# Optimization experiments

Hardware: AMD Instinct MI355X
Metric: run time of the kernel (lower is better)

## Reference

```python
import jax, jax.numpy as jnp
import numpy as np
import math

D_MODEL = 256

def setup_inputs() -> dict:
    key = jax.random.key(0)
    k1, k2, k3, k4 = jax.random.split(key, 4)
    Nq, Nh, d = 512, 100000, D_MODEL
    query_embed = jax.random.normal(k1, (Nq, d), dtype=jnp.float32)
    key_embed = jax.random.normal(k2, (Nh, d), dtype=jnp.float32)
    value_embed = jax.random.normal(k3, (Nh, d), dtype=jnp.float32)
    mask_proposals = jax.random.uniform(k4, (Nq, Nh), dtype=jnp.float32)
    return {"query_embed": query_embed, "key_embed": key_embed,
            "value_embed": value_embed, "mask_proposals": mask_proposals}

def reference(query_embed, key_embed, value_embed, mask_proposals):
    # [Nq, Nh] scores: QK^T / sqrt(d) + log(mask)
    scale = 1.0 / math.sqrt(D_MODEL)
    scores = jnp.einsum('qd,hd->qh', query_embed, key_embed) * scale
    scores = scores + jnp.log(mask_proposals)
    attn = jax.nn.softmax(scores, axis=-1)
    return jnp.einsum('qh,hd->qd', attn, value_embed)
```

## Files before the change

### kernel.cpp

```cpp
#include <hip/hip_runtime.h>
#include <hip/hip_bf16.h>

typedef __attribute__((ext_vector_type(8))) short short8;
typedef __attribute__((ext_vector_type(4))) float floatx4;
typedef __attribute__((ext_vector_type(4))) unsigned short ushort4v;

#define NQ 512
#define NH 100000
#define DM 256
#define BH 64

#define KSTR 264
#define VSTR 72
#define WSTR 72

#define MFMA_BF16(a, b, c) __builtin_amdgcn_mfma_f32_16x16x32_bf16((a), (b), (c), 0, 0, 0)

__device__ __forceinline__ unsigned short f2bf(float f) {
    union { float f; unsigned u; } v; v.f = f;
    unsigned u = v.u + 0x7fffu + ((v.u >> 16) & 1u);
    return (unsigned short)(u >> 16);
}

__global__ __launch_bounds__(512, 2)
void maskattn_phase1(const float* __restrict__ Qg,
                     const float* __restrict__ Kg,
                     const float* __restrict__ Vg,
                     const float* __restrict__ Mg,
                     float* __restrict__ numW,
                     float* __restrict__ denW,
                     int CH)
{
    __shared__ __attribute__((aligned(16))) unsigned short K_lds[64 * KSTR];
    __shared__ __attribute__((aligned(16))) unsigned short V_lds[256 * VSTR];
    __shared__ __attribute__((aligned(16))) unsigned short w_lds[128 * WSTR];
    __shared__ float den_lds[2][128];

    const int tid  = threadIdx.x;
    const int lane = tid & 63;
    const int wid  = tid >> 6;
    const int wm   = wid >> 1;
    const int wn   = wid & 1;
    const int g    = lane >> 4;
    const int l15  = lane & 15;

    const int qt    = blockIdx.x & 3;
    const int hc    = blockIdx.x >> 2;
    const int qbase = qt * 128;
    const long h0   = (long)hc * CH;
    const long hEnd = (h0 + CH < (long)NH) ? (h0 + CH) : (long)NH;

    short8 qa[2][8];
#pragma unroll
    for (int fq = 0; fq < 2; ++fq) {
        const float* qp = Qg + (size_t)(qbase + 32*wm + 16*fq + l15) * DM + 8*g;
#pragma unroll
        for (int ks = 0; ks < 8; ++ks) {
            floatx4 a = *(const floatx4*)(qp + 32*ks);
            floatx4 b = *(const floatx4*)(qp + 32*ks + 4);
            short8 fr;
            fr[0]=(short)f2bf(a[0]); fr[1]=(short)f2bf(a[1]);
            fr[2]=(short)f2bf(a[2]); fr[3]=(short)f2bf(a[3]);
            fr[4]=(short)f2bf(b[0]); fr[5]=(short)f2bf(b[1]);
            fr[6]=(short)f2bf(b[2]); fr[7]=(short)f2bf(b[3]);
            qa[fq][ks] = fr;
        }
    }

    floatx4 acc[2][8];
#pragma unroll
    for (int i = 0; i < 2; ++i)
#pragma unroll
        for (int j = 0; j < 8; ++j) {
            floatx4 z = {0.f, 0.f, 0.f, 0.f};
            acc[i][j] = z;
        }
    float dacc[8];
#pragma unroll
    for (int i = 0; i < 8; ++i) dacc[i] = 0.f;

    const int ntiles = (hEnd > h0) ? (int)((hEnd - h0 + BH - 1) / BH) : 0;

    for (int t = 0; t < ntiles; ++t) {
        const long hb = h0 + (long)t * BH;

        {
            const int hr = tid >> 3;
            const int d0 = (tid & 7) * 4;
            long krow = hb + hr; if (krow > (long)NH - 1) krow = (long)NH - 1;
            const float* kp = Kg + (size_t)krow * DM;
#pragma unroll
            for (int c = 0; c < 8; ++c) {
                const int d = d0 + 32*c;
                floatx4 v = *(const floatx4*)(kp + d);
                ushort4v p;
                p[0]=f2bf(v[0]); p[1]=f2bf(v[1]); p[2]=f2bf(v[2]); p[3]=f2bf(v[3]);
                *(ushort4v*)&K_lds[hr*KSTR + d] = p;
            }
        }
        {
            const int dcol = tid & 63;
            const int hq0  = tid >> 6;
#pragma unroll
            for (int jh = 0; jh < 2; ++jh) {
                const int hq = hq0 + 8*jh;
#pragma unroll
                for (int jd = 0; jd < 4; ++jd) {
                    const int d = dcol + 64*jd;
                    ushort4v p;
#pragma unroll
                    for (int r = 0; r < 4; ++r) {
                        long hrow = hb + 4*hq + r; if (hrow > (long)NH - 1) hrow = (long)NH - 1;
                        p[r] = f2bf(Vg[(size_t)hrow * DM + d]);
                    }
                    *(ushort4v*)&V_lds[d*VSTR + 4*hq] = p;
                }
            }
        }
        __syncthreads();

        floatx4 sf[2][2];
        {
            floatx4 z = {0.f, 0.f, 0.f, 0.f};
            sf[0][0]=z; sf[0][1]=z; sf[1][0]=z; sf[1][1]=z;
        }
#pragma unroll
        for (int ks = 0; ks < 8; ++ks) {
            short8 kb0 = *(const short8*)&K_lds[(32*wn +      l15)*KSTR + 32*ks + 8*g];
            short8 kb1 = *(const short8*)&K_lds[(32*wn + 16 + l15)*KSTR + 32*ks + 8*g];
            sf[0][0] = MFMA_BF16(qa[0][ks], kb0, sf[0][0]);
            sf[0][1] = MFMA_BF16(qa[0][ks], kb1, sf[0][1]);
            sf[1][0] = MFMA_BF16(qa[1][ks], kb0, sf[1][0]);
            sf[1][1] = MFMA_BF16(qa[1][ks], kb1, sf[1][1]);
        }

#pragma unroll
        for (int fn = 0; fn < 2; ++fn) {
            const long h = hb + 32*wn + 16*fn + l15;
            const bool valid = (h < hEnd);
#pragma unroll
            for (int fq = 0; fq < 2; ++fq) {
#pragma unroll
                for (int j = 0; j < 4; ++j) {
                    const int rloc = 32*wm + 16*fq + 4*g + j;
                    float m = valid ? Mg[(size_t)(qbase + rloc) * NH + h] : 0.f;
                    float s = sf[fq][fn][j] * 0.0625f;
                    s = (s > 60.f) ? 60.f : s;
                    float w = m * __expf(s);
                    dacc[fq*4 + j] += w;
                    w_lds[rloc*WSTR + 32*wn + 16*fn + l15] = f2bf(w);
                }
            }
        }
        __syncthreads();

#pragma unroll
        for (int ks = 0; ks < 2; ++ks) {
            short8 wa0 = *(const short8*)&w_lds[(32*wm +      l15)*WSTR + 32*ks + 8*g];
            short8 wa1 = *(const short8*)&w_lds[(32*wm + 16 + l15)*WSTR + 32*ks + 8*g];
#pragma unroll
            for (int fd = 0; fd < 8; ++fd) {
                short8 vb = *(const short8*)&V_lds[(128*wn + 16*fd + l15)*VSTR + 32*ks + 8*g];
                acc[0][fd] = MFMA_BF16(wa0, vb, acc[0][fd]);
                acc[1][fd] = MFMA_BF16(wa1, vb, acc[1][fd]);
            }
        }
        __syncthreads();
    }

#pragma unroll
    for (int r = 0; r < 8; ++r) {
        float v = dacc[r];
        v += __shfl_xor(v, 1);
        v += __shfl_xor(v, 2);
        v += __shfl_xor(v, 4);
        v += __shfl_xor(v, 8);
        if (l15 == 0) {
            const int fq = r >> 2, j = r & 3;
            den_lds[wn][32*wm + 16*fq + 4*g + j] = v;
        }
    }
    __syncthreads();
    if (tid < 128) {
        denW[(size_t)hc * NQ + qbase + tid] = den_lds[0][tid] + den_lds[1][tid];
    }

#pragma unroll
    for (int fq = 0; fq < 2; ++fq)
#pragma unroll
        for (int fd = 0; fd < 8; ++fd)
#pragma unroll
            for (int j = 0; j < 4; ++j) {
                const int qrow = qbase + 32*wm + 16*fq + 4*g + j;
                const int d    = 128*wn + 16*fd + l15;
                numW[((size_t)hc * NQ + qrow) * DM + d] = acc[fq][fd][j];
            }
}

__global__ void maskattn_reduce(const float* __restrict__ numW,
                                const float* __restrict__ denW,
                                float* __restrict__ out, int C)
{
    const int q = blockIdx.x;
    const int d = threadIdx.x;
    float sn = 0.f, sd = 0.f;
    for (int c = 0; c < C; ++c) {
        sn += numW[((size_t)c * NQ + q) * DM + d];
        sd += denW[(size_t)c * NQ + q];
    }
    out[(size_t)q * DM + d] = sn / sd;
}

extern "C" void kernel_launch(void* const* d_in, const int* in_sizes, int n_in,
                              void* d_out, int out_size, void* d_ws, size_t ws_size,
                              hipStream_t stream)
{
    const float* Qg = (const float*)d_in[0];
    const float* Kg = (const float*)d_in[1];
    const float* Vg = (const float*)d_in[2];
    const float* Mg = (const float*)d_in[3];
    float* out = (float*)d_out;

    const size_t per_chunk = (size_t)NQ * DM * sizeof(float) + (size_t)NQ * sizeof(float);
    int C = (int)(ws_size / per_chunk);
    if (C > 64) C = 64;
    float* numW;
    float* denW;
    if (C >= 1) {
        numW = (float*)d_ws;
        denW = numW + (size_t)C * NQ * DM;
    } else {
        C = 1;
        numW = out;
        denW = (float*)d_ws;
    }
    const int ch64 = (NH + 64*C - 1) / (64*C);
    const int CH = 64 * ch64;

    maskattn_phase1<<<dim3(4 * C), dim3(512), 0, stream>>>(Qg, Kg, Vg, Mg, numW, denW, CH);
    maskattn_reduce<<<dim3(NQ), dim3(DM), 0, stream>>>(numW, denW, out, C);
}
```

Before: 265.9 us.

## Shrink query tile to 64, swizzle LDS, prefetch mask, remap blocks

Query tile per block drops from 128 to 64 rows, so the grid has 8*C blocks instead of 4*C and each wave owns a single 16-row query fragment. Launch bounds move to 4 blocks per CU to raise occupancy. Padded LDS strides become XOR swizzles, which cuts LDS size and avoids bank conflicts. Mask values are loaded into registers before the K/V staging so their latency overlaps, and block IDs are remapped so neighbouring blocks share hidden chunks. The trade-off is that every K/V tile is now loaded and converted twice as often across query tiles, doubling that global traffic.

```diff
diff --git a/kernel.cpp b/kernel.cpp
--- a/kernel.cpp
+++ b/kernel.cpp
@@ -9,10 +9,7 @@
 #define NH 100000
 #define DM 256
 #define BH 64
-
-#define KSTR 264
-#define VSTR 72
-#define WSTR 72
+#define BQ 64
 
 #define MFMA_BF16(a, b, c) __builtin_amdgcn_mfma_f32_16x16x32_bf16((a), (b), (c), 0, 0, 0)
 
@@ -22,67 +19,85 @@
     return (unsigned short)(u >> 16);
 }
 
-__global__ __launch_bounds__(512, 2)
+__device__ __forceinline__ int kidx(int h, int d) { return (h * 256 + d) ^ ((h & 7) << 3); }
+__device__ __forceinline__ int vidx(int d, int h) { return (d * 64 + h) ^ ((d & 7) << 3); }
+__device__ __forceinline__ int widx(int q, int h) { return (q * 64 + h) ^ ((q & 7) << 3); }
+
+__global__ __launch_bounds__(512, 4)
 void maskattn_phase1(const float* __restrict__ Qg,
                      const float* __restrict__ Kg,
                      const float* __restrict__ Vg,
                      const float* __restrict__ Mg,
                      float* __restrict__ numW,
                      float* __restrict__ denW,
-                     int CH)
+                     int CH, int C)
 {
-    __shared__ __attribute__((aligned(16))) unsigned short K_lds[64 * KSTR];
-    __shared__ __attribute__((aligned(16))) unsigned short V_lds[256 * VSTR];
-    __shared__ __attribute__((aligned(16))) unsigned short w_lds[128 * WSTR];
-    __shared__ float den_lds[2][128];
+    __shared__ __attribute__((aligned(16))) unsigned short K_lds[64 * 256];
+    __shared__ __attribute__((aligned(16))) unsigned short V_lds[256 * 64];
+    __shared__ __attribute__((aligned(16))) unsigned short w_lds[64 * 64];
 
     const int tid  = threadIdx.x;
     const int lane = tid & 63;
     const int wid  = tid >> 6;
-    const int wm   = wid >> 1;
+    const int wq   = wid >> 1;
     const int wn   = wid & 1;
     const int g    = lane >> 4;
     const int l15  = lane & 15;
 
-    const int qt    = blockIdx.x & 3;
-    const int hc    = blockIdx.x >> 2;
-    const int qbase = qt * 128;
+    const int bid = blockIdx.x;
+    int qt, hc;
+    if ((C & 7) == 0) {
+        const int x = bid & 7;
+        const int r = bid >> 3;
+        qt = r & 7;
+        hc = x * (C >> 3) + (r >> 3);
+    } else {
+        qt = bid & 7;
+        hc = bid >> 3;
+    }
+    const int qbase = qt * BQ;
     const long h0   = (long)hc * CH;
     const long hEnd = (h0 + CH < (long)NH) ? (h0 + CH) : (long)NH;
 
-    short8 qa[2][8];
-#pragma unroll
-    for (int fq = 0; fq < 2; ++fq) {
-        const float* qp = Qg + (size_t)(qbase + 32*wm + 16*fq + l15) * DM + 8*g;
+    short8 qa[8];
+    {
+        const float* qp = Qg + (size_t)(qbase + 16 * wq + l15) * DM + 8 * g;
 #pragma unroll
         for (int ks = 0; ks < 8; ++ks) {
-            floatx4 a = *(const floatx4*)(qp + 32*ks);
-            floatx4 b = *(const floatx4*)(qp + 32*ks + 4);
+            floatx4 a = *(const floatx4*)(qp + 32 * ks);
+            floatx4 b = *(const floatx4*)(qp + 32 * ks + 4);
             short8 fr;
             fr[0]=(short)f2bf(a[0]); fr[1]=(short)f2bf(a[1]);
             fr[2]=(short)f2bf(a[2]); fr[3]=(short)f2bf(a[3]);
             fr[4]=(short)f2bf(b[0]); fr[5]=(short)f2bf(b[1]);
             fr[6]=(short)f2bf(b[2]); fr[7]=(short)f2bf(b[3]);
-            qa[fq][ks] = fr;
-        }
-    }
-
-    floatx4 acc[2][8];
-#pragma unroll
-    for (int i = 0; i < 2; ++i)
-#pragma unroll
-        for (int j = 0; j < 8; ++j) {
-            floatx4 z = {0.f, 0.f, 0.f, 0.f};
-            acc[i][j] = z;
-        }
-    float dacc[8];
-#pragma unroll
-    for (int i = 0; i < 8; ++i) dacc[i] = 0.f;
+            qa[ks] = fr;
+        }
+    }
+
+    floatx4 acc[8];
+#pragma unroll
+    for (int i = 0; i < 8; ++i) {
+        floatx4 z = {0.f, 0.f, 0.f, 0.f};
+        acc[i] = z;
+    }
+    float dacc[4] = {0.f, 0.f, 0.f, 0.f};
 
     const int ntiles = (hEnd > h0) ? (int)((hEnd - h0 + BH - 1) / BH) : 0;
 
     for (int t = 0; t < ntiles; ++t) {
         const long hb = h0 + (long)t * BH;
+
+        float mreg[2][4];
+#pragma unroll
+        for (int fn = 0; fn < 2; ++fn) {
+            const long h = hb + 32 * wn + 16 * fn + l15;
+            const bool valid = (h < hEnd);
+#pragma unroll
+            for (int j = 0; j < 4; ++j) {
+                mreg[fn][j] = valid ? Mg[(size_t)(qbase + 16 * wq + 4 * g + j) * NH + h] : 0.f;
+            }
+        }
 
         {
             const int hr = tid >> 3;
@@ -91,11 +106,11 @@
             const float* kp = Kg + (size_t)krow * DM;
 #pragma unroll
             for (int c = 0; c < 8; ++c) {
-                const int d = d0 + 32*c;
+                const int d = d0 + 32 * c;
                 floatx4 v = *(const floatx4*)(kp + d);
                 ushort4v p;
                 p[0]=f2bf(v[0]); p[1]=f2bf(v[1]); p[2]=f2bf(v[2]); p[3]=f2bf(v[3]);
-                *(ushort4v*)&K_lds[hr*KSTR + d] = p;
+                *(ushort4v*)&K_lds[kidx(hr, d)] = p;
             }
         }
         {
@@ -103,98 +118,85 @@
             const int hq0  = tid >> 6;
 #pragma unroll
             for (int jh = 0; jh < 2; ++jh) {
-                const int hq = hq0 + 8*jh;
+                const int hq = hq0 + 8 * jh;
 #pragma unroll
                 for (int jd = 0; jd < 4; ++jd) {
-                    const int d = dcol + 64*jd;
+                    const int d = dcol + 64 * jd;
                     ushort4v p;
 #pragma unroll
                     for (int r = 0; r < 4; ++r) {
-                        long hrow = hb + 4*hq + r; if (hrow > (long)NH - 1) hrow = (long)NH - 1;
+                        long hrow = hb + 4 * hq + r; if (hrow > (long)NH - 1) hrow = (long)NH - 1;
                         p[r] = f2bf(Vg[(size_t)hrow * DM + d]);
                     }
-                    *(ushort4v*)&V_lds[d*VSTR + 4*hq] = p;
+                    *(ushort4v*)&V_lds[vidx(d, 4 * hq)] = p;
                 }
             }
         }
         __syncthreads();
 
-        floatx4 sf[2][2];
+        floatx4 sf[2];
         {
             floatx4 z = {0.f, 0.f, 0.f, 0.f};
-            sf[0][0]=z; sf[0][1]=z; sf[1][0]=z; sf[1][1]=z;
+            sf[0] = z; sf[1] = z;
         }
 #pragma unroll
         for (int ks = 0; ks < 8; ++ks) {
-            short8 kb0 = *(const short8*)&K_lds[(32*wn +      l15)*KSTR + 32*ks + 8*g];
-            short8 kb1 = *(const short8*)&K_lds[(32*wn + 16 + l15)*KSTR + 32*ks + 8*g];
-            sf[0][0] = MFMA_BF16(qa[0][ks], kb0, sf[0][0]);
-            sf[0][1] = MFMA_BF16(qa[0][ks], kb1, sf[0][1]);
-            sf[1][0] = MFMA_BF16(qa[1][ks], kb0, sf[1][0]);
-            sf[1][1] = MFMA_BF16(qa[1][ks], kb1, sf[1][1]);
+            short8 kb0 = *(const short8*)&K_lds[kidx(32 * wn +      l15, 32 * ks + 8 * g)];
+            short8 kb1 = *(const short8*)&K_lds[kidx(32 * wn + 16 + l15, 32 * ks + 8 * g)];
+            sf[0] = MFMA_BF16(qa[ks], kb0, sf[0]);
+            sf[1] = MFMA_BF16(qa[ks], kb1, sf[1]);
         }
 
 #pragma unroll
         for (int fn = 0; fn < 2; ++fn) {
-            const long h = hb + 32*wn + 16*fn + l15;
-            const bool valid = (h < hEnd);
-#pragma unroll
-            for (int fq = 0; fq < 2; ++fq) {
-#pragma unroll
-                for (int j = 0; j < 4; ++j) {
-                    const int rloc = 32*wm + 16*fq + 4*g + j;
-                    float m = valid ? Mg[(size_t)(qbase + rloc) * NH + h] : 0.f;
-                    float s = sf[fq][fn][j] * 0.0625f;
-                    s = (s > 60.f) ? 60.f : s;
-                    float w = m * __expf(s);
-                    dacc[fq*4 + j] += w;
-                    w_lds[rloc*WSTR + 32*wn + 16*fn + l15] = f2bf(w);
-                }
+#pragma unroll
+            for (int j = 0; j < 4; ++j) {
+                const int rloc = 16 * wq + 4 * g + j;
+                float s = sf[fn][j] * 0.0625f;
+                s = (s > 60.f) ? 60.f : s;
+                float w = mreg[fn][j] * __expf(s);
+                dacc[j] += w;
+                w_lds[widx(rloc, 32 * wn + 16 * fn + l15)] = f2bf(w);
             }
         }
         __syncthreads();
 
 #pragma unroll
         for (int ks = 0; ks < 2; ++ks) {
-            short8 wa0 = *(const short8*)&w_lds[(32*wm +      l15)*WSTR + 32*ks + 8*g];
-            short8 wa1 = *(const short8*)&w_lds[(32*wm + 16 + l15)*WSTR + 32*ks + 8*g];
+            short8 wa = *(const short8*)&w_lds[widx(16 * wq + l15, 32 * ks + 8 * g)];
 #pragma unroll
             for (int fd = 0; fd < 8; ++fd) {
-                short8 vb = *(const short8*)&V_lds[(128*wn + 16*fd + l15)*VSTR + 32*ks + 8*g];
-                acc[0][fd] = MFMA_BF16(wa0, vb, acc[0][fd]);
-                acc[1][fd] = MFMA_BF16(wa1, vb, acc[1][fd]);
+                short8 vb = *(const short8*)&V_lds[vidx(128 * wn + 16 * fd + l15, 32 * ks + 8 * g)];
+                acc[fd] = MFMA_BF16(wa, vb, acc[fd]);
             }
         }
         __syncthreads();
     }
 
-#pragma unroll
-    for (int r = 0; r < 8; ++r) {
-        float v = dacc[r];
+    __syncthreads();
+    float* dshare = (float*)w_lds;
+#pragma unroll
+    for (int j = 0; j < 4; ++j) {
+        float v = dacc[j];
         v += __shfl_xor(v, 1);
         v += __shfl_xor(v, 2);
         v += __shfl_xor(v, 4);
         v += __shfl_xor(v, 8);
-        if (l15 == 0) {
-            const int fq = r >> 2, j = r & 3;
-            den_lds[wn][32*wm + 16*fq + 4*g + j] = v;
-        }
+        if (l15 == 0) dshare[wn * 64 + 16 * wq + 4 * g + j] = v;
     }
     __syncthreads();
-    if (tid < 128) {
-        denW[(size_t)hc * NQ + qbase + tid] = den_lds[0][tid] + den_lds[1][tid];
-    }
-
-#pragma unroll
-    for (int fq = 0; fq < 2; ++fq)
-#pragma unroll
-        for (int fd = 0; fd < 8; ++fd)
-#pragma unroll
-            for (int j = 0; j < 4; ++j) {
-                const int qrow = qbase + 32*wm + 16*fq + 4*g + j;
-                const int d    = 128*wn + 16*fd + l15;
-                numW[((size_t)hc * NQ + qrow) * DM + d] = acc[fq][fd][j];
-            }
+    if (tid < BQ) {
+        denW[(size_t)hc * NQ + qbase + tid] = dshare[tid] + dshare[64 + tid];
+    }
+
+#pragma unroll
+    for (int fd = 0; fd < 8; ++fd)
+#pragma unroll
+        for (int j = 0; j < 4; ++j) {
+            const int qrow = qbase + 16 * wq + 4 * g + j;
+            const int d    = 128 * wn + 16 * fd + l15;
+            numW[((size_t)hc * NQ + qrow) * DM + d] = acc[fd][j];
+        }
 }
 
 __global__ void maskattn_reduce(const float* __restrict__ numW,
@@ -234,9 +236,9 @@
         numW = out;
         denW = (float*)d_ws;
     }
-    const int ch64 = (NH + 64*C - 1) / (64*C);
+    const int ch64 = (NH + 64 * C - 1) / (64 * C);
     const int CH = 64 * ch64;
 
-    maskattn_phase1<<<dim3(4 * C), dim3(512), 0, stream>>>(Qg, Kg, Vg, Mg, numW, denW, CH);
+    maskattn_phase1<<<dim3((NQ / BQ) * C), dim3(512), 0, stream>>>(Qg, Kg, Vg, Mg, numW, denW, CH, C);
     maskattn_reduce<<<dim3(NQ), dim3(DM), 0, stream>>>(numW, denW, out, C);
 }
```

Measured after the change: 507.9 us. 1.91x slower.

## Double-buffer K/V tiles with register prefetch and XOR-swizzled LDS layout

Applied to the files above, without the earlier changes.

The K/V loads and mask loads for the next tile are now issued into registers before the current tile's two MFMA stages, then written to a second LDS buffer after the PV MFMAs. Global memory latency can then overlap with compute, and the previous per-tile load-then-sync stall goes away. Padded LDS strides are replaced by XOR swizzles to avoid bank conflicts. Blocks are also remapped so that consecutive block IDs spread across h-chunks. The cost is higher register pressure (kreg, vreg and two mask arrays) and double the K/V LDS, which may lower occupancy below the two blocks per CU requested by launch bounds.

```diff
diff --git a/kernel.cpp b/kernel.cpp
--- a/kernel.cpp
+++ b/kernel.cpp
@@ -9,10 +9,7 @@
 #define NH 100000
 #define DM 256
 #define BH 64
-
-#define KSTR 264
-#define VSTR 72
-#define WSTR 72
+#define BQ 128
 
 #define MFMA_BF16(a, b, c) __builtin_amdgcn_mfma_f32_16x16x32_bf16((a), (b), (c), 0, 0, 0)
 
@@ -20,6 +17,71 @@
     union { float f; unsigned u; } v; v.f = f;
     unsigned u = v.u + 0x7fffu + ((v.u >> 16) & 1u);
     return (unsigned short)(u >> 16);
+}
+
+__device__ __forceinline__ int kidx(int h, int d) { return (h * 256 + d) ^ ((h & 7) << 3); }
+__device__ __forceinline__ int vidx(int d, int h) { return (d * 64 + h) ^ ((d & 7) << 3); }
+__device__ __forceinline__ int widx(int q, int h) { return (q * 64 + h) ^ ((q & 7) << 3); }
+
+__device__ __forceinline__ void issue_kv(const float* __restrict__ Kg,
+                                         const float* __restrict__ Vg,
+                                         long hb, int tid,
+                                         floatx4* kreg, float* vreg)
+{
+    const int khr = tid >> 3, kd0 = (tid & 7) * 4;
+    long krow = hb + khr; if (krow > (long)NH - 1) krow = (long)NH - 1;
+    const float* kp = Kg + (size_t)krow * DM;
+#pragma unroll
+    for (int c = 0; c < 8; ++c) kreg[c] = *(const floatx4*)(kp + kd0 + 32 * c);
+
+    const int vd = tid & 63, vh0 = tid >> 6;
+#pragma unroll
+    for (int jh = 0; jh < 2; ++jh)
+#pragma unroll
+        for (int r = 0; r < 4; ++r) {
+            long vrow = hb + 4 * (vh0 + 8 * jh) + r; if (vrow > (long)NH - 1) vrow = (long)NH - 1;
+            const float* vp = Vg + (size_t)vrow * DM + vd;
+#pragma unroll
+            for (int jd = 0; jd < 4; ++jd)
+                vreg[jh * 16 + jd * 4 + r] = vp[64 * jd];
+        }
+}
+
+__device__ __forceinline__ void write_kv(unsigned short* Kb, unsigned short* Vb,
+                                         int tid, const floatx4* kreg, const float* vreg)
+{
+    const int khr = tid >> 3, kd0 = (tid & 7) * 4;
+#pragma unroll
+    for (int c = 0; c < 8; ++c) {
+        floatx4 v = kreg[c];
+        ushort4v p;
+        p[0] = f2bf(v[0]); p[1] = f2bf(v[1]); p[2] = f2bf(v[2]); p[3] = f2bf(v[3]);
+        *(ushort4v*)&Kb[kidx(khr, kd0 + 32 * c)] = p;
+    }
+    const int vd = tid & 63, vh0 = tid >> 6;
+#pragma unroll
+    for (int jh = 0; jh < 2; ++jh)
+#pragma unroll
+        for (int jd = 0; jd < 4; ++jd) {
+            ushort4v p;
+#pragma unroll
+            for (int r = 0; r < 4; ++r) p[r] = f2bf(vreg[jh * 16 + jd * 4 + r]);
+            *(ushort4v*)&Vb[vidx(vd + 64 * jd, 4 * (vh0 + 8 * jh))] = p;
+        }
+}
+
+__device__ __forceinline__ void issue_mask(const float* __restrict__ Mg, long hb,
+                                           int qrow0, int wn, int g, int l15, float* m)
+{
+#pragma unroll
+    for (int fn = 0; fn < 2; ++fn) {
+        long h = hb + 32 * wn + 16 * fn + l15; if (h > (long)NH - 1) h = (long)NH - 1;
+#pragma unroll
+        for (int fq = 0; fq < 2; ++fq)
+#pragma unroll
+            for (int j = 0; j < 4; ++j)
+                m[fn * 8 + fq * 4 + j] = Mg[(size_t)(qrow0 + 16 * fq + 4 * g + j) * NH + h];
+    }
 }
 
 __global__ __launch_bounds__(512, 2)
@@ -29,12 +91,11 @@
                      const float* __restrict__ Mg,
                      float* __restrict__ numW,
                      float* __restrict__ denW,
-                     int CH)
-{
-    __shared__ __attribute__((aligned(16))) unsigned short K_lds[64 * KSTR];
-    __shared__ __attribute__((aligned(16))) unsigned short V_lds[256 * VSTR];
-    __shared__ __attribute__((aligned(16))) unsigned short w_lds[128 * WSTR];
-    __shared__ float den_lds[2][128];
+                     int CH, int C)
+{
+    __shared__ __attribute__((aligned(16))) unsigned short K_lds[2][64 * 256];
+    __shared__ __attribute__((aligned(16))) unsigned short V_lds[2][64 * 256];
+    __shared__ __attribute__((aligned(16))) unsigned short w_lds[128 * 64];
 
     const int tid  = threadIdx.x;
     const int lane = tid & 63;
@@ -44,20 +105,30 @@
     const int g    = lane >> 4;
     const int l15  = lane & 15;
 
-    const int qt    = blockIdx.x & 3;
-    const int hc    = blockIdx.x >> 2;
-    const int qbase = qt * 128;
+    const int bid = blockIdx.x;
+    int qt, hc;
+    if ((C & 7) == 0) {
+        const int x = bid & 7;
+        const int r = bid >> 3;
+        qt = r & 3;
+        hc = x * (C >> 3) + (r >> 2);
+    } else {
+        qt = bid & 3;
+        hc = bid >> 2;
+    }
+    const int qbase = qt * BQ;
     const long h0   = (long)hc * CH;
     const long hEnd = (h0 + CH < (long)NH) ? (h0 + CH) : (long)NH;
+    const int qrow0 = qbase + 32 * wm;
 
     short8 qa[2][8];
 #pragma unroll
     for (int fq = 0; fq < 2; ++fq) {
-        const float* qp = Qg + (size_t)(qbase + 32*wm + 16*fq + l15) * DM + 8*g;
+        const float* qp = Qg + (size_t)(qrow0 + 16 * fq + l15) * DM + 8 * g;
 #pragma unroll
         for (int ks = 0; ks < 8; ++ks) {
-            floatx4 a = *(const floatx4*)(qp + 32*ks);
-            floatx4 b = *(const floatx4*)(qp + 32*ks + 4);
+            floatx4 a = *(const floatx4*)(qp + 32 * ks);
+            floatx4 b = *(const floatx4*)(qp + 32 * ks + 4);
             short8 fr;
             fr[0]=(short)f2bf(a[0]); fr[1]=(short)f2bf(a[1]);
             fr[2]=(short)f2bf(a[2]); fr[3]=(short)f2bf(a[3]);
@@ -71,103 +142,85 @@
 #pragma unroll
     for (int i = 0; i < 2; ++i)
 #pragma unroll
-        for (int j = 0; j < 8; ++j) {
-            floatx4 z = {0.f, 0.f, 0.f, 0.f};
-            acc[i][j] = z;
-        }
+        for (int j = 0; j < 8; ++j) { floatx4 z = {0.f,0.f,0.f,0.f}; acc[i][j] = z; }
     float dacc[8];
 #pragma unroll
     for (int i = 0; i < 8; ++i) dacc[i] = 0.f;
 
     const int ntiles = (hEnd > h0) ? (int)((hEnd - h0 + BH - 1) / BH) : 0;
 
-    for (int t = 0; t < ntiles; ++t) {
-        const long hb = h0 + (long)t * BH;
-
-        {
-            const int hr = tid >> 3;
-            const int d0 = (tid & 7) * 4;
-            long krow = hb + hr; if (krow > (long)NH - 1) krow = (long)NH - 1;
-            const float* kp = Kg + (size_t)krow * DM;
-#pragma unroll
-            for (int c = 0; c < 8; ++c) {
-                const int d = d0 + 32*c;
-                floatx4 v = *(const floatx4*)(kp + d);
-                ushort4v p;
-                p[0]=f2bf(v[0]); p[1]=f2bf(v[1]); p[2]=f2bf(v[2]); p[3]=f2bf(v[3]);
-                *(ushort4v*)&K_lds[hr*KSTR + d] = p;
-            }
-        }
-        {
-            const int dcol = tid & 63;
-            const int hq0  = tid >> 6;
-#pragma unroll
-            for (int jh = 0; jh < 2; ++jh) {
-                const int hq = hq0 + 8*jh;
-#pragma unroll
-                for (int jd = 0; jd < 4; ++jd) {
-                    const int d = dcol + 64*jd;
-                    ushort4v p;
-#pragma unroll
-                    for (int r = 0; r < 4; ++r) {
-                        long hrow = hb + 4*hq + r; if (hrow > (long)NH - 1) hrow = (long)NH - 1;
-                        p[r] = f2bf(Vg[(size_t)hrow * DM + d]);
+    if (ntiles > 0) {
+        floatx4 kreg[8];
+        float   vreg[32];
+        float   mcur[16], mnext[16];
+
+        issue_kv(Kg, Vg, h0, tid, kreg, vreg);
+        issue_mask(Mg, h0, qrow0, wn, g, l15, mcur);
+        write_kv(K_lds[0], V_lds[0], tid, kreg, vreg);
+        __syncthreads();
+
+        int cur = 0;
+        for (int t = 0; t < ntiles; ++t) {
+            const long hb = h0 + (long)t * BH;
+
+            issue_kv(Kg, Vg, hb + BH, tid, kreg, vreg);
+            issue_mask(Mg, hb + BH, qrow0, wn, g, l15, mnext);
+
+            const unsigned short* Kc = K_lds[cur];
+            floatx4 sf[2][2];
+            { floatx4 z = {0.f,0.f,0.f,0.f}; sf[0][0]=z; sf[0][1]=z; sf[1][0]=z; sf[1][1]=z; }
+#pragma unroll
+            for (int ks = 0; ks < 8; ++ks) {
+                short8 kb0 = *(const short8*)&Kc[kidx(32 * wn +      l15, 32 * ks + 8 * g)];
+                short8 kb1 = *(const short8*)&Kc[kidx(32 * wn + 16 + l15, 32 * ks + 8 * g)];
+                sf[0][0] = MFMA_BF16(qa[0][ks], kb0, sf[0][0]);
+                sf[0][1] = MFMA_BF16(qa[0][ks], kb1, sf[0][1]);
+                sf[1][0] = MFMA_BF16(qa[1][ks], kb0, sf[1][0]);
+                sf[1][1] = MFMA_BF16(qa[1][ks], kb1, sf[1][1]);
+            }
+
+#pragma unroll
+            for (int fn = 0; fn < 2; ++fn) {
+                const long h = hb + 32 * wn + 16 * fn + l15;
+                const bool valid = (h < hEnd);
+#pragma unroll
+                for (int fq = 0; fq < 2; ++fq)
+#pragma unroll
+                    for (int j = 0; j < 4; ++j) {
+                        const int rloc = 32 * wm + 16 * fq + 4 * g + j;
+                        float m = valid ? mcur[fn * 8 + fq * 4 + j] : 0.f;
+                        float s = sf[fq][fn][j] * 0.0625f;
+                        s = (s > 60.f) ? 60.f : s;
+                        float w = m * __expf(s);
+                        dacc[fq * 4 + j] += w;
+                        w_lds[widx(rloc, 32 * wn + 16 * fn + l15)] = f2bf(w);
                     }
-                    *(ushort4v*)&V_lds[d*VSTR + 4*hq] = p;
+            }
+            __syncthreads();
+
+            const unsigned short* Vc = V_lds[cur];
+#pragma unroll
+            for (int ks = 0; ks < 2; ++ks) {
+                short8 wa0 = *(const short8*)&w_lds[widx(32 * wm +      l15, 32 * ks + 8 * g)];
+                short8 wa1 = *(const short8*)&w_lds[widx(32 * wm + 16 + l15, 32 * ks + 8 * g)];
+#pragma unroll
+                for (int fd = 0; fd < 8; ++fd) {
+                    short8 vb = *(const short8*)&Vc[vidx(128 * wn + 16 * fd + l15, 32 * ks + 8 * g)];
+                    acc[0][fd] = MFMA_BF16(wa0, vb, acc[0][fd]);
+                    acc[1][fd] = MFMA_BF16(wa1, vb, acc[1][fd]);
                 }
             }
-        }
-        __syncthreads();
-
-        floatx4 sf[2][2];
-        {
-            floatx4 z = {0.f, 0.f, 0.f, 0.f};
-            sf[0][0]=z; sf[0][1]=z; sf[1][0]=z; sf[1][1]=z;
-        }
-#pragma unroll
-        for (int ks = 0; ks < 8; ++ks) {
-            short8 kb0 = *(const short8*)&K_lds[(32*wn +      l15)*KSTR + 32*ks + 8*g];
-            short8 kb1 = *(const short8*)&K_lds[(32*wn + 16 + l15)*KSTR + 32*ks + 8*g];
-            sf[0][0] = MFMA_BF16(qa[0][ks], kb0, sf[0][0]);
-            sf[0][1] = MFMA_BF16(qa[0][ks], kb1, sf[0][1]);
-            sf[1][0] = MFMA_BF16(qa[1][ks], kb0, sf[1][0]);
-            sf[1][1] = MFMA_BF16(qa[1][ks], kb1, sf[1][1]);
-        }
-
-#pragma unroll
-        for (int fn = 0; fn < 2; ++fn) {
-            const long h = hb + 32*wn + 16*fn + l15;
-            const bool valid = (h < hEnd);
-#pragma unroll
-            for (int fq = 0; fq < 2; ++fq) {
-#pragma unroll
-                for (int j = 0; j < 4; ++j) {
-                    const int rloc = 32*wm + 16*fq + 4*g + j;
-                    float m = valid ? Mg[(size_t)(qbase + rloc) * NH + h] : 0.f;
-                    float s = sf[fq][fn][j] * 0.0625f;
-                    s = (s > 60.f) ? 60.f : s;
-                    float w = m * __expf(s);
-                    dacc[fq*4 + j] += w;
-                    w_lds[rloc*WSTR + 32*wn + 16*fn + l15] = f2bf(w);
-                }
-            }
-        }
-        __syncthreads();
-
-#pragma unroll
-        for (int ks = 0; ks < 2; ++ks) {
-            short8 wa0 = *(const short8*)&w_lds[(32*wm +      l15)*WSTR + 32*ks + 8*g];
-            short8 wa1 = *(const short8*)&w_lds[(32*wm + 16 + l15)*WSTR + 32*ks + 8*g];
-#pragma unroll
-            for (int fd = 0; fd < 8; ++fd) {
-                short8 vb = *(const short8*)&V_lds[(128*wn + 16*fd + l15)*VSTR + 32*ks + 8*g];
-                acc[0][fd] = MFMA_BF16(wa0, vb, acc[0][fd]);
-                acc[1][fd] = MFMA_BF16(wa1, vb, acc[1][fd]);
-            }
-        }
-        __syncthreads();
-    }
-
+
+            write_kv(K_lds[cur ^ 1], V_lds[cur ^ 1], tid, kreg, vreg);
+#pragma unroll
+            for (int i = 0; i < 16; ++i) mcur[i] = mnext[i];
+            __syncthreads();
+            cur ^= 1;
+        }
+    }
+
+    __syncthreads();
+    float* dshare = (float*)w_lds;
 #pragma unroll
     for (int r = 0; r < 8; ++r) {
         float v = dacc[r];
@@ -177,12 +230,12 @@
         v += __shfl_xor(v, 8);
         if (l15 == 0) {
             const int fq = r >> 2, j = r & 3;
-            den_lds[wn][32*wm + 16*fq + 4*g + j] = v;
+            dshare[wn * 128 + 32 * wm + 16 * fq + 4 * g + j] = v;
         }
     }
     __syncthreads();
-    if (tid < 128) {
-        denW[(size_t)hc * NQ + qbase + tid] = den_lds[0][tid] + den_lds[1][tid];
+    if (tid < BQ) {
+        denW[(size_t)hc * NQ + qbase + tid] = dshare[tid] + dshare[128 + tid];
     }
 
 #pragma unroll
@@ -191,8 +244,8 @@
         for (int fd = 0; fd < 8; ++fd)
 #pragma unroll
             for (int j = 0; j < 4; ++j) {
-                const int qrow = qbase + 32*wm + 16*fq + 4*g + j;
-                const int d    = 128*wn + 16*fd + l15;
+                const int qrow = qbase + 32 * wm + 16 * fq + 4 * g + j;
+                const int d    = 128 * wn + 16 * fd + l15;
                 numW[((size_t)hc * NQ + qrow) * DM + d] = acc[fq][fd][j];
             }
 }
@@ -234,9 +287,9 @@
         numW = out;
         denW = (float*)d_ws;
     }
-    const int ch64 = (NH + 64*C - 1) / (64*C);
+    const int ch64 = (NH + 64 * C - 1) / (64 * C);
     const int CH = 64 * ch64;
 
-    maskattn_phase1<<<dim3(4 * C), dim3(512), 0, stream>>>(Qg, Kg, Vg, Mg, numW, denW, CH);
+    maskattn_phase1<<<dim3((NQ / BQ) * C), dim3(512), 0, stream>>>(Qg, Kg, Vg, Mg, numW, denW, CH, C);
     maskattn_reduce<<<dim3(NQ), dim3(DM), 0, stream>>>(numW, denW, out, C);
 }
```

New measurement: 665.0 us. 150% more time.
